# Kernel optimization log

Hardware: AMD Instinct MI355X
Metric: run time of the kernel (lower is better)

Reference implementation:

```python
import jax, jax.numpy as jnp
import numpy as np

B, S, D, H = 2, 2048, 1024, 16
DH = D // H  # 64


def setup_inputs() -> dict:
    key = jax.random.key(0)
    ks = jax.random.split(key, 12)
    scale = 0.02
    q = jax.random.normal(ks[0], (B, S, D), dtype=jnp.float32)
    k = jax.random.normal(ks[1], (B, S, D), dtype=jnp.float32)
    v = jax.random.normal(ks[2], (B, S, D), dtype=jnp.float32)
    # CTRL-style causal mask: 1.0 above the diagonal (positions to mask), 0.0 elsewhere
    mask = jnp.triu(jnp.ones((S, S), dtype=jnp.float32), k=1)
    Wq = jax.random.normal(ks[3], (D, D), dtype=jnp.float32) * scale
    bq = jnp.zeros((D,), dtype=jnp.float32)
    Wk = jax.random.normal(ks[4], (D, D), dtype=jnp.float32) * scale
    bk = jnp.zeros((D,), dtype=jnp.float32)
    Wv = jax.random.normal(ks[5], (D, D), dtype=jnp.float32) * scale
    bv = jnp.zeros((D,), dtype=jnp.float32)
    Wo = jax.random.normal(ks[6], (D, D), dtype=jnp.float32) * scale
    bo = jnp.zeros((D,), dtype=jnp.float32)
    return {"q": q, "k": k, "v": v, "mask": mask,
            "Wq": Wq, "bq": bq, "Wk": Wk, "bk": bk,
            "Wv": Wv, "bv": bv, "Wo": Wo, "bo": bo}


def _split_heads(x):
    # [B, S, D] -> [B, H, S, DH]
    b, s, _ = x.shape
    return x.reshape(b, s, H, DH).transpose(0, 2, 1, 3)


def reference(q, k, v, mask, Wq, bq, Wk, bk, Wv, bv, Wo, bo):
    # QKV projections
    qh = _split_heads(q @ Wq + bq)  # [B, H, S, DH]
    kh = _split_heads(k @ Wk + bk)
    vh = _split_heads(v @ Wv + bv)
    # scaled dot-product attention with CTRL mask convention (mask * -1e4 added)
    scores = jnp.einsum('bhqd,bhkd->bhqk', qh, kh) / jnp.sqrt(jnp.float32(DH))
    scores = scores + mask * -10000.0  # mask broadcasts [S,S] -> [B,H,S,S]
    weights = jax.nn.softmax(scores, axis=-1)
    ctx = jnp.einsum('bhqk,bhkd->bhqd', weights, vh)  # [B, H, S, DH]
    ctx = ctx.transpose(0, 2, 1, 3).reshape(q.shape[0], -1, D)  # [B, S, D]
    return ctx @ Wo + bo
```

## Files before the change

### kernel.cpp

```cpp
#include <hip/hip_runtime.h>
#include <stdint.h>

typedef unsigned short u16;
typedef __attribute__((ext_vector_type(8))) short bf16x8;
typedef __attribute__((ext_vector_type(4))) float f32x4;
typedef __attribute__((ext_vector_type(4))) unsigned short u16x4;

#define C_SCALE 0.1803368801111204f
#define C_MASK  -14426.950408889634f

__device__ __forceinline__ float bf2f(u16 x) {
  union { uint32_t u; float f; } v; v.u = ((uint32_t)x) << 16; return v.f;
}
__device__ __forceinline__ u16 f2bf(float f) {
  union { float f; uint32_t u; } v; v.f = f;
  return (u16)((v.u + 0x7FFFu + ((v.u >> 16) & 1u)) >> 16);
}

__device__ __forceinline__ void load_lds16(const void* g, void* l) {
  __builtin_amdgcn_global_load_lds(
      (const __attribute__((address_space(1))) uint32_t*)g,
      (__attribute__((address_space(3))) uint32_t*)l, 16, 0, 0);
}

__device__ __forceinline__ uint32_t pack_trunc(uint32_t f_even, uint32_t f_odd) {
  return __builtin_amdgcn_perm(f_odd, f_even, 0x07060302u);
}

__device__ __forceinline__ bool detect_bf16(const u16* __restrict__ q) {
  int lane = threadIdx.x & 63;
  u16 w = q[lane * 4];
  int e = (w >> 7) & 0xFF;
  unsigned long long b = __ballot(e >= 96 && e <= 159);
  return __popcll(b) >= 48;
}

__device__ __forceinline__ void wait_vm(int n) {
  switch (n) {
    case 0:  __builtin_amdgcn_s_waitcnt(0x0F70); break;
    case 2:  __builtin_amdgcn_s_waitcnt(0x0F72); break;
    case 4:  __builtin_amdgcn_s_waitcnt(0x0F74); break;
    case 6:  __builtin_amdgcn_s_waitcnt(0x0F76); break;
    case 8:  __builtin_amdgcn_s_waitcnt(0x0F78); break;
    case 12: __builtin_amdgcn_s_waitcnt(0x0F7C); break;
    case 16: __builtin_amdgcn_s_waitcnt(0x4F70); break;
    default: __builtin_amdgcn_s_waitcnt(0x4F74); break;
  }
}
__device__ __forceinline__ void wait_lgkm0() { __builtin_amdgcn_s_waitcnt(0xC07F); }
#define SBAR()  __builtin_amdgcn_s_barrier()
#define SCHED() __builtin_amdgcn_sched_barrier(0)

__global__ __launch_bounds__(256) void transpose_all(const u16* __restrict__ W0,
                                                     const u16* __restrict__ W1,
                                                     const u16* __restrict__ W2,
                                                     const u16* __restrict__ W3,
                                                     u16* __restrict__ WTb,
                                                     const u16* __restrict__ qprobe) {
  constexpr int D = 1024;
  __shared__ u16 tile[64][72];
  const int z = blockIdx.z;
  const u16* W = z == 0 ? W0 : (z == 1 ? W1 : (z == 2 ? W2 : W3));
  u16* WT = WTb + (size_t)z * D * D;
  const bool isbf = detect_bf16(qprobe);
  const int x0 = blockIdx.x * 64, y0 = blockIdx.y * 64;
  const int t = threadIdx.x;
  const int r = t >> 3;
  const int c8 = (t & 7) << 3;
#pragma unroll
  for (int hh = 0; hh < 2; ++hh) {
    int row = r + hh * 32;
    if (isbf) {
      *(uint4*)&tile[row][c8] = *(const uint4*)&W[(size_t)(y0 + row) * D + x0 + c8];
    } else {
      const float* Wf = (const float*)W;
      float4 f0 = *(const float4*)&Wf[(size_t)(y0 + row) * D + x0 + c8];
      float4 f1 = *(const float4*)&Wf[(size_t)(y0 + row) * D + x0 + c8 + 4];
      u16 tmp[8] = {f2bf(f0.x), f2bf(f0.y), f2bf(f0.z), f2bf(f0.w),
                    f2bf(f1.x), f2bf(f1.y), f2bf(f1.z), f2bf(f1.w)};
      *(uint4*)&tile[row][c8] = *(uint4*)tmp;
    }
  }
  __syncthreads();
#pragma unroll
  for (int hh = 0; hh < 2; ++hh) {
    int row = r + hh * 32;
    u16 tmp[8];
#pragma unroll
    for (int i = 0; i < 8; ++i) tmp[i] = tile[c8 + i][row];
    *(uint4*)&WT[(size_t)(x0 + row) * D + y0 + c8] = *(uint4*)tmp;
  }
}


__device__ __forceinline__ void stage_tile32(const u16* __restrict__ src, int row0,
                                             int k0, u16* dst, int wave, int lane) {
  constexpr int K = 1024;
#pragma unroll
  for (int p = 0; p < 2; ++p) {
    int seg = wave * 2 + p;
    int r = seg * 16 + (lane >> 2);
    int c = lane & 3;
    int cg = c ^ ((r >> 1) & 3);
    load_lds16(&src[(size_t)(row0 + r) * K + k0 + cg * 8], dst + seg * 512);
  }
}

#define FRAG_READS(Ab, Bb)                                                    \
  _Pragma("unroll") for (int i = 0; i < 4; ++i) {                             \
    int r = wm + 16 * i + lr;                                                 \
    af[i] = *(const bf16x8*)&(Ab)[r * 32 + ((quad ^ ((r >> 1) & 3)) * 8)];    \
  }                                                                           \
  _Pragma("unroll") for (int jj = 0; jj < 4; ++jj) {                          \
    int r = wn + 16 * jj + lr;                                                \
    bff[jj] = *(const bf16x8*)&(Bb)[r * 32 + ((quad ^ ((r >> 1) & 3)) * 8)];  \
  }

#define MFMA16()                                                              \
  _Pragma("unroll") for (int i = 0; i < 4; ++i)                               \
  _Pragma("unroll") for (int jj = 0; jj < 4; ++jj)                            \
      acc[i][jj] = __builtin_amdgcn_mfma_f32_16x16x32_bf16(af[i], bff[jj],    \
                                                           acc[i][jj], 0, 0, 0);

template <int NS>
__device__ __forceinline__ void kloop_dma(const u16* __restrict__ A,
                                          const u16* __restrict__ BT,
                                          int m0, int n0, u16* As, u16* Bs,
                                          int wave, int lane, f32x4 (&acc)[4][4]) {
  const int quad = lane >> 4, lr = lane & 15;
  const int wm = (wave & 1) * 64, wn = (wave >> 1) * 64;
  auto stage = [&](int t, int buf) {
    stage_tile32(A, m0, t * 32, As + buf * 4096, wave, lane);
    stage_tile32(BT, n0, t * 32, Bs + buf * 4096, wave, lane);
  };
#pragma unroll
  for (int s = 0; s < NS; ++s) stage(s, s);
  int buf = 0;
#pragma unroll 1
  for (int t = 0; t < 32; ++t) {
    SCHED();
    int rem = 31 - t;
    wait_vm(rem >= NS - 1 ? 4 * (NS - 1) : 4 * rem);
    SBAR();
    SCHED();
    bf16x8 af[4], bff[4];
    const u16* Ab = As + buf * 4096;
    const u16* Bb = Bs + buf * 4096;
    FRAG_READS(Ab, Bb)
    wait_lgkm0();
    SCHED();
    SBAR();
    if (t + NS < 32) stage(t + NS, buf);
    MFMA16()
    buf = buf + 1 == NS ? 0 : buf + 1;
  }
}

__device__ __forceinline__ void kloop_f32(const float* __restrict__ Af,
                                          const u16* __restrict__ BT,
                                          int m0, int n0, u16* As, u16* Bs,
                                          int tid, f32x4 (&acc)[4][4]) {
  constexpr int K = 1024;
  const int wave = tid >> 6, lane = tid & 63;
  const int quad = lane >> 4, lr = lane & 15;
  const int wm = (wave & 1) * 64, wn = (wave >> 1) * 64;
  const int ar = tid >> 1, ah = tid & 1;
  const uint32_t* Au = (const uint32_t*)Af;
  uint4 ra0[4], ra1[4];
  auto loadA = [&](int t, uint4 (&r)[4]) {
    const uint32_t* p = &Au[(size_t)(m0 + ar) * K + t * 32 + ah * 16];
    r[0] = *(const uint4*)(p + 0);
    r[1] = *(const uint4*)(p + 4);
    r[2] = *(const uint4*)(p + 8);
    r[3] = *(const uint4*)(p + 12);
  };
  auto writeA = [&](int buf, uint4 (&rr)[4]) {
    uint4 o0, o1;
    o0.x = pack_trunc(rr[0].x, rr[0].y); o0.y = pack_trunc(rr[0].z, rr[0].w);
    o0.z = pack_trunc(rr[1].x, rr[1].y); o0.w = pack_trunc(rr[1].z, rr[1].w);
    o1.x = pack_trunc(rr[2].x, rr[2].y); o1.y = pack_trunc(rr[2].z, rr[2].w);
    o1.z = pack_trunc(rr[3].x, rr[3].y); o1.w = pack_trunc(rr[3].z, rr[3].w);
    int sw = (ar >> 1) & 3;
    int c0 = (2 * ah) ^ sw, c1 = (2 * ah + 1) ^ sw;
    *(uint4*)&As[buf * 4096 + ar * 32 + c0 * 8] = o0;
    *(uint4*)&As[buf * 4096 + ar * 32 + c1 * 8] = o1;
  };
  auto stageB = [&](int t, int buf) {
    stage_tile32(BT, n0, t * 32, Bs + buf * 4096, wave, lane);
  };
  stageB(0, 0); loadA(0, ra0);
  stageB(1, 1); loadA(1, ra1);
  SCHED(); wait_vm(6); writeA(0, ra0);
  stageB(2, 2); loadA(2, ra0);
  SCHED(); wait_vm(6); writeA(1, ra1);
  loadA(3, ra1);
  SCHED(); wait_vm(4); writeA(2, ra0);

  int buf = 0;
#pragma unroll 1
  for (int j = 0; j < 14; ++j) {
#pragma unroll
    for (int half = 0; half < 2; ++half) {
      const int t = 2 * j + half;
      SCHED();
      wait_vm(16);
      SBAR();
      SCHED();
      bf16x8 af[4], bff[4];
      const u16* Ab = As + buf * 4096;
      const u16* Bb = Bs + buf * 4096;
      FRAG_READS(Ab, Bb)
      wait_lgkm0();
      SCHED();
      SBAR();
      stageB(t + 3, buf);
      if (half == 0) { loadA(t + 4, ra0); SCHED(); wait_vm(6); writeA(buf, ra1); }
      else           { loadA(t + 4, ra1); SCHED(); wait_vm(6); writeA(buf, ra0); }
      MFMA16()
      buf = buf + 1 == 3 ? 0 : buf + 1;
    }
  }
  {
    SCHED(); wait_vm(16); SBAR(); SCHED();
    bf16x8 af[4], bff[4];
    const u16 *Ab = As + buf * 4096, *Bb = Bs + buf * 4096;
    FRAG_READS(Ab, Bb)
    wait_lgkm0(); SCHED(); SBAR();
    stageB(31, buf);
    SCHED(); wait_vm(2); writeA(buf, ra1);
    MFMA16()
    buf = 2;
  }
  {
    SCHED(); wait_vm(12); SBAR(); SCHED();
    bf16x8 af[4], bff[4];
    const u16 *Ab = As + buf * 4096, *Bb = Bs + buf * 4096;
    FRAG_READS(Ab, Bb)
    MFMA16()
    buf = 0;
  }
  {
    SCHED(); wait_vm(6); SBAR(); SCHED();
    bf16x8 af[4], bff[4];
    const u16 *Ab = As + buf * 4096, *Bb = Bs + buf * 4096;
    FRAG_READS(Ab, Bb)
    MFMA16()
    buf = 1;
  }
  {
    SCHED(); wait_vm(0); SBAR(); SCHED();
    bf16x8 af[4], bff[4];
    const u16 *Ab = As + buf * 4096, *Bb = Bs + buf * 4096;
    FRAG_READS(Ab, Bb)
    MFMA16()
  }
}

__global__ __launch_bounds__(256, 3) void gemm_qkv(
    const u16* __restrict__ A0, const u16* __restrict__ A1, const u16* __restrict__ A2,
    const u16* __restrict__ WTb,
    const u16* __restrict__ b0, const u16* __restrict__ b1, const u16* __restrict__ b2,
    u16* __restrict__ Chb) {
  __shared__ u16 As[3 * 4096];
  __shared__ u16 Bs[3 * 4096];
  const int z = blockIdx.y;
  const u16* A = z == 0 ? A0 : (z == 1 ? A1 : A2);
  const u16* bias = z == 0 ? b0 : (z == 1 ? b1 : b2);
  const u16* BT = WTb + (size_t)z * 1024 * 1024;
  u16* C = Chb + (size_t)z * 4 * 1024 * 1024;
  const bool isbf = detect_bf16(A0);
  const int tid = threadIdx.x;
  const int wave = tid >> 6, lane = tid & 63;
  const int quad = lane >> 4, lr = lane & 15;
  const int f = blockIdx.x;
  const int n0 = (f >> 5) * 128;
  const int m0 = (f & 31) * 128;
  const int wm = (wave & 1) * 64, wn = (wave >> 1) * 64;

  f32x4 acc[4][4] = {};
  if (isbf) kloop_dma<3>(A, BT, m0, n0, As, Bs, wave, lane, acc);
  else      kloop_f32((const float*)A, BT, m0, n0, As, Bs, tid, acc);

#pragma unroll
  for (int i = 0; i < 4; ++i) {
#pragma unroll
    for (int jj = 0; jj < 4; ++jj) {
      int n = n0 + wn + 16 * jj + lr;
      float bv = isbf ? bf2f(bias[n]) : ((const float*)bias)[n];
#pragma unroll
      for (int r = 0; r < 4; ++r) {
        int m = m0 + wm + 16 * i + quad * 4 + r;
        float val = acc[i][jj][r] + bv;
        int b = m >> 11, s = m & 2047, h = n >> 6, dh = n & 63;
        C[((size_t)(b * 16 + h) * 2048 + s) * 64 + dh] = f2bf(val);
      }
    }
  }
}

__global__ __launch_bounds__(256) void gemm_out(const u16* __restrict__ A,
                                                const u16* __restrict__ BT,
                                                const u16* __restrict__ bias,
                                                u16* __restrict__ C,
                                                const u16* __restrict__ qprobe) {
  constexpr int N = 1024;
  __shared__ u16 As[6 * 4096];
  __shared__ u16 Bs[6 * 4096];
  const bool isbf = detect_bf16(qprobe);
  const int tid = threadIdx.x;
  const int wave = tid >> 6, lane = tid & 63;
  const int quad = lane >> 4, lr = lane & 15;
  const int f = blockIdx.x;
  const int n0 = (f >> 5) * 128;
  const int m0 = (f & 31) * 128;
  const int wm = (wave & 1) * 64, wn = (wave >> 1) * 64;

  f32x4 acc[4][4] = {};
  kloop_dma<6>(A, BT, m0, n0, As, Bs, wave, lane, acc);

#pragma unroll
  for (int i = 0; i < 4; ++i) {
#pragma unroll
    for (int jj = 0; jj < 4; ++jj) {
      int n = n0 + wn + 16 * jj + lr;
      float bv = isbf ? bf2f(bias[n]) : ((const float*)bias)[n];
#pragma unroll
      for (int r = 0; r < 4; ++r) {
        int m = m0 + wm + 16 * i + quad * 4 + r;
        float val = acc[i][jj][r] + bv;
        size_t idx = (size_t)m * N + n;
        if (isbf) C[idx] = f2bf(val);
        else ((float*)C)[idx] = val;
      }
    }
  }
}

__global__ __launch_bounds__(256, 2) void attn_fwd(const u16* __restrict__ Qh,
                                                   const u16* __restrict__ Kh,
                                                   const u16* __restrict__ Vh,
                                                   u16* __restrict__ ctx) {
  constexpr int S = 2048, DH = 64, Dm = 1024;
  __shared__ u16 Ks[2][64 * 64];
  __shared__ u16 Vt[2][64 * 72];
  __shared__ u16 Pl[4][16 * 72];
  const int tid = threadIdx.x;
  const int wave = tid >> 6, lane = tid & 63;
  const int quad = lane >> 4, lr = lane & 15;
  const int bh = blockIdx.y;
  const int bx = (int)blockIdx.x;
  const size_t base = (size_t)bh * S * DH;
  const u16* Q = Qh + base;
  const u16* Kp = Kh + base;
  const u16* Vp = Vh + base;
  u16* Plw = Pl[wave];
  const int b = bh >> 4, h = bh & 15;

  const int vkey2 = (tid & 31) * 2, vd8 = (tid >> 5) * 8;
  uint4 va, vbr;

  auto stageK = [&](int kt, int kbuf) {
#pragma unroll
    for (int p = 0; p < 2; ++p) {
      int s = (wave * 2 + p) * 64 + lane;
      int r = s >> 3, cg = (s & 7) ^ (r & 7);
      load_lds16(&Kp[(size_t)(kt + r) * DH + cg * 8], &Ks[kbuf][(wave * 2 + p) * 512]);
    }
  };
  auto loadV = [&](int kt) {
    va  = *(const uint4*)&Vp[(size_t)(kt + vkey2) * DH + vd8];
    vbr = *(const uint4*)&Vp[(size_t)(kt + vkey2 + 1) * DH + vd8];
  };
  auto writeV = [&](int vbuf) {
    const u16* pa = (const u16*)&va;
    const u16* pb = (const u16*)&vbr;
#pragma unroll
    for (int i = 0; i < 8; ++i) {
      uint32_t pair = (uint32_t)pa[i] | ((uint32_t)pb[i] << 16);
      *(uint32_t*)&Vt[vbuf][(vd8 + i) * 72 + vkey2] = pair;
    }
  };

  int kb = 0, vb = 0;
  for (int ph = 0; ph < 2; ++ph) {
    const int qt = ph == 0 ? (31 - bx) : bx;
    const int q0 = qt * 64;
    const int nt = qt + 1;
    const int qg = q0 + wave * 16 + lr;

    bf16x8 aQ[2];
#pragma unroll
    for (int s = 0; s < 2; ++s)
      aQ[s] = *(const bf16x8*)&Q[(size_t)(q0 + wave * 16 + lr) * DH + s * 32 + quad * 8];

    f32x4 o[4] = {};
    float m_i = -1.0e5f;
    float l_i = 0.f;

    __syncthreads();
    stageK(0, kb);
    loadV(0);
    writeV(vb);
    if (nt > 1) loadV(64);

    for (int it = 0; it < nt; ++it) {
      const int kt = it * 64;
      __syncthreads();

      bf16x8 aK[4][2], bV[4][2];
#pragma unroll
      for (int t = 0; t < 4; ++t) {
        int r = t * 16 + lr;
#pragma unroll
        for (int s = 0; s < 2; ++s) {
          int ch = (s * 4 + quad) ^ (r & 7);
          aK[t][s] = *(const bf16x8*)&Ks[kb][r * 64 + ch * 8];
        }
      }
#pragma unroll
      for (int c = 0; c < 4; ++c)
#pragma unroll
        for (int s = 0; s < 2; ++s)
          bV[c][s] = *(const bf16x8*)&Vt[vb][(c * 16 + lr) * 72 + s * 32 + quad * 8];

      if (it + 1 < nt) {
        stageK(kt + 64, kb ^ 1);
        writeV(vb ^ 1);
        if (it + 2 < nt) loadV(kt + 128);
      }

      f32x4 sc[4];
#pragma unroll
      for (int t = 0; t < 4; ++t) {
        f32x4 zz = {0.f, 0.f, 0.f, 0.f};
        zz = __builtin_amdgcn_mfma_f32_16x16x32_bf16(aK[t][0], aQ[0], zz, 0, 0, 0);
        zz = __builtin_amdgcn_mfma_f32_16x16x32_bf16(aK[t][1], aQ[1], zz, 0, 0, 0);
        sc[t] = zz;
      }

      const bool diag = (it == nt - 1);
      float v[4][4];
      float mx = -1.0e5f;
      if (diag) {
#pragma unroll
        for (int t = 0; t < 4; ++t)
#pragma unroll
          for (int r = 0; r < 4; ++r) {
            int kg = kt + t * 16 + quad * 4 + r;
            float x = sc[t][r] * C_SCALE + ((kg > qg) ? C_MASK : 0.f);
            v[t][r] = x;
            mx = fmaxf(mx, x);
          }
      } else {
#pragma unroll
        for (int t = 0; t < 4; ++t)
#pragma unroll
          for (int r = 0; r < 4; ++r) {
            float x = sc[t][r] * C_SCALE;
            v[t][r] = x;
            mx = fmaxf(mx, x);
          }
      }
      mx = fmaxf(mx, __shfl_xor(mx, 16));
      mx = fmaxf(mx, __shfl_xor(mx, 32));
      float m_new = fmaxf(m_i, mx);
      float sum = 0.f;
      u16 pb16[4][4];
#pragma unroll
      for (int t = 0; t < 4; ++t)
#pragma unroll
        for (int r = 0; r < 4; ++r) {
          float p = exp2f(v[t][r] - m_new);
          sum += p;
          pb16[t][r] = f2bf(p);
        }
      sum += __shfl_xor(sum, 16);
      sum += __shfl_xor(sum, 32);
      float alpha = exp2f(m_i - m_new);
      l_i = l_i * alpha + sum;
      m_i = m_new;
#pragma unroll
      for (int t = 0; t < 4; ++t) {
        u16x4 w = {pb16[t][0], pb16[t][1], pb16[t][2], pb16[t][3]};
        *(u16x4*)&Plw[lr * 72 + t * 16 + quad * 4] = w;
      }
#pragma unroll
      for (int r = 0; r < 4; ++r) {
        float ab = __shfl(alpha, quad * 4 + r);
#pragma unroll
        for (int c = 0; c < 4; ++c) o[c][r] *= ab;
      }
      asm volatile("s_waitcnt lgkmcnt(0)" ::: "memory");
      bf16x8 aP[2];
#pragma unroll
      for (int s = 0; s < 2; ++s)
        aP[s] = *(const bf16x8*)&Plw[lr * 72 + s * 32 + quad * 8];
#pragma unroll
      for (int c = 0; c < 4; ++c)
#pragma unroll
        for (int s = 0; s < 2; ++s)
          o[c] = __builtin_amdgcn_mfma_f32_16x16x32_bf16(aP[s], bV[c][s], o[c], 0, 0, 0);
      kb ^= 1; vb ^= 1;
    }

    float linv = 1.f / l_i;
#pragma unroll
    for (int r = 0; r < 4; ++r) {
      float lb = __shfl(linv, quad * 4 + r);
      int s = q0 + wave * 16 + quad * 4 + r;
      size_t orow = ((size_t)b * S + s) * Dm + h * DH;
#pragma unroll
      for (int c = 0; c < 4; ++c) ctx[orow + c * 16 + lr] = f2bf(o[c][r] * lb);
    }
  }
}

extern "C" void kernel_launch(void* const* d_in, const int* in_sizes, int n_in,
                              void* d_out, int out_size, void* d_ws, size_t ws_size,
                              hipStream_t stream) {
  const u16* q  = (const u16*)d_in[0];
  const u16* k  = (const u16*)d_in[1];
  const u16* v  = (const u16*)d_in[2];
  const u16* Wq = (const u16*)d_in[4];
  const u16* bq = (const u16*)d_in[5];
  const u16* Wk = (const u16*)d_in[6];
  const u16* bk = (const u16*)d_in[7];
  const u16* Wv = (const u16*)d_in[8];
  const u16* bv = (const u16*)d_in[9];
  const u16* Wo = (const u16*)d_in[10];
  const u16* bo = (const u16*)d_in[11];
  u16* out = (u16*)d_out;

  constexpr size_t M1 = 1024 * 1024;
  u16* ws = (u16*)d_ws;
  u16* WT  = ws;
  u16* Qh  = WT + 4 * M1;
  u16* ctx = Qh + 12 * M1;

  dim3 tb(256);
  transpose_all<<<dim3(16, 16, 4), tb, 0, stream>>>(Wq, Wk, Wv, Wo, WT, q);
  gemm_qkv<<<dim3(256, 3), tb, 0, stream>>>(q, k, v, WT, bq, bk, bv, Qh);
  attn_fwd<<<dim3(16, 32), tb, 0, stream>>>(Qh, Qh + 4 * M1, Qh + 8 * M1, ctx);
  gemm_out<<<dim3(256), tb, 0, stream>>>(ctx, WT + 3 * M1, bo, out, q);
}
```

Baseline: 268.5 us.

## Simplify GEMM pipelines to double-buffered syncthreads loops and halve gemm_out M-tile

Replaces the hand-tuned multi-stage (3/6 buffer) GEMM k-loops, which used explicit waitcnt and sched barriers, with plain double-buffered loops synchronized by __syncthreads. gemm_out now uses 64x128 tiles with 512 blocks and launch bounds of 2 blocks per CU, giving more blocks on the device and lower LDS use per block. The trade is less latency hiding per block, since __syncthreads forces full waits on the DMA loads, and more reliance on occupancy to cover memory latency.

```diff
diff --git a/kernel.cpp b/kernel.cpp
--- a/kernel.cpp
+++ b/kernel.cpp
@@ -34,22 +34,6 @@
   unsigned long long b = __ballot(e >= 96 && e <= 159);
   return __popcll(b) >= 48;
 }
-
-__device__ __forceinline__ void wait_vm(int n) {
-  switch (n) {
-    case 0:  __builtin_amdgcn_s_waitcnt(0x0F70); break;
-    case 2:  __builtin_amdgcn_s_waitcnt(0x0F72); break;
-    case 4:  __builtin_amdgcn_s_waitcnt(0x0F74); break;
-    case 6:  __builtin_amdgcn_s_waitcnt(0x0F76); break;
-    case 8:  __builtin_amdgcn_s_waitcnt(0x0F78); break;
-    case 12: __builtin_amdgcn_s_waitcnt(0x0F7C); break;
-    case 16: __builtin_amdgcn_s_waitcnt(0x4F70); break;
-    default: __builtin_amdgcn_s_waitcnt(0x4F74); break;
-  }
-}
-__device__ __forceinline__ void wait_lgkm0() { __builtin_amdgcn_s_waitcnt(0xC07F); }
-#define SBAR()  __builtin_amdgcn_s_barrier()
-#define SCHED() __builtin_amdgcn_sched_barrier(0)
 
 __global__ __launch_bounds__(256) void transpose_all(const u16* __restrict__ W0,
                                                      const u16* __restrict__ W1,
@@ -122,44 +106,44 @@
       acc[i][jj] = __builtin_amdgcn_mfma_f32_16x16x32_bf16(af[i], bff[jj],    \
                                                            acc[i][jj], 0, 0, 0);
 
-template <int NS>
-__device__ __forceinline__ void kloop_dma(const u16* __restrict__ A,
-                                          const u16* __restrict__ BT,
-                                          int m0, int n0, u16* As, u16* Bs,
-                                          int wave, int lane, f32x4 (&acc)[4][4]) {
+__device__ __forceinline__ void kloop2_dma(const u16* __restrict__ A,
+                                           const u16* __restrict__ BT,
+                                           int m0, int n0, u16* As, u16* Bs,
+                                           int wave, int lane, f32x4 (&acc)[4][4]) {
   const int quad = lane >> 4, lr = lane & 15;
   const int wm = (wave & 1) * 64, wn = (wave >> 1) * 64;
   auto stage = [&](int t, int buf) {
     stage_tile32(A, m0, t * 32, As + buf * 4096, wave, lane);
     stage_tile32(BT, n0, t * 32, Bs + buf * 4096, wave, lane);
   };
-#pragma unroll
-  for (int s = 0; s < NS; ++s) stage(s, s);
-  int buf = 0;
+  stage(0, 0);
+  __syncthreads();
 #pragma unroll 1
-  for (int t = 0; t < 32; ++t) {
-    SCHED();
-    int rem = 31 - t;
-    wait_vm(rem >= NS - 1 ? 4 * (NS - 1) : 4 * rem);
-    SBAR();
-    SCHED();
-    bf16x8 af[4], bff[4];
-    const u16* Ab = As + buf * 4096;
-    const u16* Bb = Bs + buf * 4096;
-    FRAG_READS(Ab, Bb)
-    wait_lgkm0();
-    SCHED();
-    SBAR();
-    if (t + NS < 32) stage(t + NS, buf);
-    MFMA16()
-    buf = buf + 1 == NS ? 0 : buf + 1;
-  }
-}
-
-__device__ __forceinline__ void kloop_f32(const float* __restrict__ Af,
-                                          const u16* __restrict__ BT,
-                                          int m0, int n0, u16* As, u16* Bs,
-                                          int tid, f32x4 (&acc)[4][4]) {
+  for (int j = 0; j < 16; ++j) {
+    const int t0 = 2 * j;
+    {
+      stage(t0 + 1, 1);
+      bf16x8 af[4], bff[4];
+      const u16 *Ab = As, *Bb = Bs;
+      FRAG_READS(Ab, Bb)
+      MFMA16()
+      __syncthreads();
+    }
+    {
+      if (t0 + 2 < 32) stage(t0 + 2, 0);
+      bf16x8 af[4], bff[4];
+      const u16 *Ab = As + 4096, *Bb = Bs + 4096;
+      FRAG_READS(Ab, Bb)
+      MFMA16()
+      __syncthreads();
+    }
+  }
+}
+
+__device__ __forceinline__ void kloop2_f32(const float* __restrict__ Af,
+                                           const u16* __restrict__ BT,
+                                           int m0, int n0, u16* As, u16* Bs,
+                                           int tid, f32x4 (&acc)[4][4]) {
   constexpr int K = 1024;
   const int wave = tid >> 6, lane = tid & 63;
   const int quad = lane >> 4, lr = lane & 15;
@@ -188,71 +172,33 @@
   auto stageB = [&](int t, int buf) {
     stage_tile32(BT, n0, t * 32, Bs + buf * 4096, wave, lane);
   };
-  stageB(0, 0); loadA(0, ra0);
-  stageB(1, 1); loadA(1, ra1);
-  SCHED(); wait_vm(6); writeA(0, ra0);
-  stageB(2, 2); loadA(2, ra0);
-  SCHED(); wait_vm(6); writeA(1, ra1);
-  loadA(3, ra1);
-  SCHED(); wait_vm(4); writeA(2, ra0);
-
-  int buf = 0;
+  loadA(0, ra0);
+  stageB(0, 0);
+  loadA(1, ra1);
+  writeA(0, ra0);
+  __syncthreads();
 #pragma unroll 1
-  for (int j = 0; j < 14; ++j) {
-#pragma unroll
-    for (int half = 0; half < 2; ++half) {
-      const int t = 2 * j + half;
-      SCHED();
-      wait_vm(16);
-      SBAR();
-      SCHED();
+  for (int j = 0; j < 16; ++j) {
+    const int t0 = 2 * j;
+    {
+      stageB(t0 + 1, 1);
+      writeA(1, ra1);
+      if (t0 + 2 < 32) loadA(t0 + 2, ra0);
       bf16x8 af[4], bff[4];
-      const u16* Ab = As + buf * 4096;
-      const u16* Bb = Bs + buf * 4096;
+      const u16 *Ab = As, *Bb = Bs;
       FRAG_READS(Ab, Bb)
-      wait_lgkm0();
-      SCHED();
-      SBAR();
-      stageB(t + 3, buf);
-      if (half == 0) { loadA(t + 4, ra0); SCHED(); wait_vm(6); writeA(buf, ra1); }
-      else           { loadA(t + 4, ra1); SCHED(); wait_vm(6); writeA(buf, ra0); }
       MFMA16()
-      buf = buf + 1 == 3 ? 0 : buf + 1;
-    }
-  }
-  {
-    SCHED(); wait_vm(16); SBAR(); SCHED();
-    bf16x8 af[4], bff[4];
-    const u16 *Ab = As + buf * 4096, *Bb = Bs + buf * 4096;
-    FRAG_READS(Ab, Bb)
-    wait_lgkm0(); SCHED(); SBAR();
-    stageB(31, buf);
-    SCHED(); wait_vm(2); writeA(buf, ra1);
-    MFMA16()
-    buf = 2;
-  }
-  {
-    SCHED(); wait_vm(12); SBAR(); SCHED();
-    bf16x8 af[4], bff[4];
-    const u16 *Ab = As + buf * 4096, *Bb = Bs + buf * 4096;
-    FRAG_READS(Ab, Bb)
-    MFMA16()
-    buf = 0;
-  }
-  {
-    SCHED(); wait_vm(6); SBAR(); SCHED();
-    bf16x8 af[4], bff[4];
-    const u16 *Ab = As + buf * 4096, *Bb = Bs + buf * 4096;
-    FRAG_READS(Ab, Bb)
-    MFMA16()
-    buf = 1;
-  }
-  {
-    SCHED(); wait_vm(0); SBAR(); SCHED();
-    bf16x8 af[4], bff[4];
-    const u16 *Ab = As + buf * 4096, *Bb = Bs + buf * 4096;
-    FRAG_READS(Ab, Bb)
-    MFMA16()
+      __syncthreads();
+    }
+    {
+      if (t0 + 2 < 32) { stageB(t0 + 2, 0); writeA(0, ra0); }
+      if (t0 + 3 < 32) loadA(t0 + 3, ra1);
+      bf16x8 af[4], bff[4];
+      const u16 *Ab = As + 4096, *Bb = Bs + 4096;
+      FRAG_READS(Ab, Bb)
+      MFMA16()
+      __syncthreads();
+    }
   }
 }
 
@@ -261,8 +207,8 @@
     const u16* __restrict__ WTb,
     const u16* __restrict__ b0, const u16* __restrict__ b1, const u16* __restrict__ b2,
     u16* __restrict__ Chb) {
-  __shared__ u16 As[3 * 4096];
-  __shared__ u16 Bs[3 * 4096];
+  __shared__ u16 As[2 * 4096];
+  __shared__ u16 Bs[2 * 4096];
   const int z = blockIdx.y;
   const u16* A = z == 0 ? A0 : (z == 1 ? A1 : A2);
   const u16* bias = z == 0 ? b0 : (z == 1 ? b1 : b2);
@@ -278,8 +224,8 @@
   const int wm = (wave & 1) * 64, wn = (wave >> 1) * 64;
 
   f32x4 acc[4][4] = {};
-  if (isbf) kloop_dma<3>(A, BT, m0, n0, As, Bs, wave, lane, acc);
-  else      kloop_f32((const float*)A, BT, m0, n0, As, Bs, tid, acc);
+  if (isbf) kloop2_dma(A, BT, m0, n0, As, Bs, wave, lane, acc);
+  else      kloop2_f32((const float*)A, BT, m0, n0, As, Bs, tid, acc);
 
 #pragma unroll
   for (int i = 0; i < 4; ++i) {
@@ -298,28 +244,69 @@
   }
 }
 
-__global__ __launch_bounds__(256) void gemm_out(const u16* __restrict__ A,
-                                                const u16* __restrict__ BT,
-                                                const u16* __restrict__ bias,
-                                                u16* __restrict__ C,
-                                                const u16* __restrict__ qprobe) {
-  constexpr int N = 1024;
-  __shared__ u16 As[6 * 4096];
-  __shared__ u16 Bs[6 * 4096];
+__global__ __launch_bounds__(256, 2) void gemm_out(const u16* __restrict__ A,
+                                                   const u16* __restrict__ BT,
+                                                   const u16* __restrict__ bias,
+                                                   u16* __restrict__ C,
+                                                   const u16* __restrict__ qprobe) {
+  constexpr int N = 1024, K = 1024;
+  __shared__ u16 As[2 * 2048];
+  __shared__ u16 Bs[2 * 4096];
   const bool isbf = detect_bf16(qprobe);
   const int tid = threadIdx.x;
   const int wave = tid >> 6, lane = tid & 63;
   const int quad = lane >> 4, lr = lane & 15;
   const int f = blockIdx.x;
-  const int n0 = (f >> 5) * 128;
-  const int m0 = (f & 31) * 128;
-  const int wm = (wave & 1) * 64, wn = (wave >> 1) * 64;
-
-  f32x4 acc[4][4] = {};
-  kloop_dma<6>(A, BT, m0, n0, As, Bs, wave, lane, acc);
-
-#pragma unroll
-  for (int i = 0; i < 4; ++i) {
+  const int n0 = (f >> 6) * 128;
+  const int m0 = (f & 63) * 64;
+  const int wm = (wave & 1) * 32, wn = (wave >> 1) * 64;
+
+  auto stage = [&](int t, int buf) {
+    {
+      int r = wave * 16 + (lane >> 2);
+      int c = lane & 3;
+      int cg = c ^ ((r >> 1) & 3);
+      load_lds16(&A[(size_t)(m0 + r) * K + t * 32 + cg * 8],
+                 As + buf * 2048 + wave * 512);
+    }
+    stage_tile32(BT, n0, t * 32, Bs + buf * 4096, wave, lane);
+  };
+
+  f32x4 acc[2][4] = {};
+  stage(0, 0);
+  __syncthreads();
+#pragma unroll 1
+  for (int j = 0; j < 16; ++j) {
+    const int t0 = 2 * j;
+#pragma unroll
+    for (int half = 0; half < 2; ++half) {
+      const int t = t0 + half;
+      if (t + 1 < 32) stage(t + 1, (t + 1) & 1);
+      bf16x8 af[2], bff[4];
+      const u16* Ab = As + (t & 1) * 2048;
+      const u16* Bb = Bs + (t & 1) * 4096;
+#pragma unroll
+      for (int i = 0; i < 2; ++i) {
+        int r = wm + 16 * i + lr;
+        af[i] = *(const bf16x8*)&Ab[r * 32 + ((quad ^ ((r >> 1) & 3)) * 8)];
+      }
+#pragma unroll
+      for (int jj = 0; jj < 4; ++jj) {
+        int r = wn + 16 * jj + lr;
+        bff[jj] = *(const bf16x8*)&Bb[r * 32 + ((quad ^ ((r >> 1) & 3)) * 8)];
+      }
+#pragma unroll
+      for (int i = 0; i < 2; ++i)
+#pragma unroll
+        for (int jj = 0; jj < 4; ++jj)
+          acc[i][jj] =
+              __builtin_amdgcn_mfma_f32_16x16x32_bf16(af[i], bff[jj], acc[i][jj], 0, 0, 0);
+      __syncthreads();
+    }
+  }
+
+#pragma unroll
+  for (int i = 0; i < 2; ++i) {
 #pragma unroll
     for (int jj = 0; jj < 4; ++jj) {
       int n = n0 + wn + 16 * jj + lr;
@@ -541,5 +528,5 @@
   transpose_all<<<dim3(16, 16, 4), tb, 0, stream>>>(Wq, Wk, Wv, Wo, WT, q);
   gemm_qkv<<<dim3(256, 3), tb, 0, stream>>>(q, k, v, WT, bq, bk, bv, Qh);
   attn_fwd<<<dim3(16, 32), tb, 0, stream>>>(Qh, Qh + 4 * M1, Qh + 8 * M1, ctx);
-  gemm_out<<<dim3(256), tb, 0, stream>>>(ctx, WT + 3 * M1, bo, out, q);
-}
+  gemm_out<<<dim3(512), tb, 0, stream>>>(ctx, WT + 3 * M1, bo, out, q);
+}
```

Measured after the change: 254.1 us. -5.4%, faster.
